# Performance work log

Measured on AMD Instinct MI355X. Metric: run time of the kernel, lower is better.

Reference implementation:

```python
import jax, jax.numpy as jnp
import numpy as np

BITS = 4            # bits per quantized weight
NPACK = 8           # 32-bit container / 4-bit values
CBITS = 32          # compression dtype bit width (int32)
GROUP = 128         # quantization group size along in_features
IN = 4096
OUT = 11008
BATCH = 32


def _dequant(packed_weight, scale):
    # Unpack signed int4 values: (p << (32 - 4*(e+1))) >> 28, arithmetic shift
    # sign-extends, matching the torch recover() path for weight_dtype=int8.
    e = jnp.arange(NPACK, dtype=jnp.int32)                      # [8]
    shifted = (packed_weight[:, :, None] << (CBITS - BITS * (e + 1))) >> (CBITS - BITS)  # [O, I/8, 8]
    w_int = shifted.reshape(OUT, IN).astype(jnp.int8)           # signed int4 in int8
    # Per-group scale: reshape to [O*I/GROUP, GROUP] * [O*I/GROUP, 1]
    w = w_int.astype(jnp.float32).reshape(-1, GROUP) * scale.reshape(-1, 1)
    return w.reshape(OUT, IN)


def setup_inputs() -> dict:
    key = jax.random.key(0)
    k1, k2, k3, k4 = jax.random.split(key, 4)
    x = jax.random.normal(k1, (BATCH, IN), dtype=jnp.float32)
    packed_weight = jax.random.randint(
        k2, (OUT, IN // NPACK), jnp.iinfo(jnp.int32).min, jnp.iinfo(jnp.int32).max,
        dtype=jnp.int32)
    scale = jax.random.uniform(k3, (OUT, IN // GROUP), dtype=jnp.float32,
                               minval=0.001, maxval=0.02)
    bias = jax.random.normal(k4, (OUT,), dtype=jnp.float32)
    return {"x": x, "packed_weight": packed_weight, "scale": scale, "bias": bias}


def reference(x, packed_weight, scale, bias):
    W = _dequant(packed_weight, scale)      # [OUT, IN] fp32
    return x @ W.T + bias                    # F.linear(x, W, bias)
```

## Files before the change

kernel.cpp:

```cpp
#include <hip/hip_runtime.h>

#define IN_F   4096
#define OUT_F  11008
#define BATCH  32
#define NG     32
#define PACKS  512

typedef __bf16 bf16x8_t __attribute__((ext_vector_type(8)));
typedef float  floatx4_t __attribute__((ext_vector_type(4)));

__global__ __launch_bounds__(256) void prep_x(const float* __restrict__ x,
                                              unsigned short* __restrict__ xp) {
  int c  = blockIdx.x * 256 + threadIdx.x;
  int mm = c & 31;
  int k0 = ((c >> 5) & 3) * 32 + ((c >> 7) & 3) * 8 + (c >> 9) * 128;
  const float* src = x + mm * IN_F + k0;
  float4 f0 = *(const float4*)(src);
  float4 f1 = *(const float4*)(src + 4);
  float v[8] = {f0.x, f0.y, f0.z, f0.w, f1.x, f1.y, f1.z, f1.w};
  union { unsigned short s[8]; uint4 u; } r;
#pragma unroll
  for (int j = 0; j < 8; ++j) {
    unsigned int u = __float_as_uint(v[j]);
    unsigned int rnd = ((u >> 16) & 1u) + 0x7fffu;
    r.s[j] = (unsigned short)((u + rnd) >> 16);
  }
  *(uint4*)(xp + c * 8) = r.u;
}

__device__ inline bf16x8_t unpack8(int p) {
  union { unsigned short u[8]; bf16x8_t v; } r;
#pragma unroll
  for (int j = 0; j < 8; ++j) {
    int nib = (p << (28 - 4 * j)) >> 28;
    float f = (float)nib;
    r.u[j] = (unsigned short)(__float_as_uint(f) >> 16);
  }
  return r.v;
}

__device__ inline bf16x8_t load_frag(const unsigned short* p) {
  union { uint4 u; bf16x8_t v; } x;
  x.u = *(const uint4*)p;
  return x.v;
}

__global__ __launch_bounds__(256) void init_out(const float* __restrict__ bias,
                                                float* __restrict__ out) {
  int i = blockIdx.x * 256 + threadIdx.x;
  int e = i << 2;
  int row = e / OUT_F, o = e % OUT_F;
  float4 b = *(const float4*)(bias + o);
  *(float4*)(out + row * OUT_F + o) = b;
}

__global__ __launch_bounds__(256) void wql_part(
    const int* __restrict__ pw, const float* __restrict__ scale,
    const unsigned short* __restrict__ xp, float* __restrict__ out) {
  __shared__ float lds[4][BATCH * 32];

  const int tid = threadIdx.x;
  const int l   = tid & 63;
  const int w   = tid >> 6;
  const int col = l & 15;
  const int q   = l >> 4;
  const int n0  = blockIdx.x * 32;
  const int kc  = blockIdx.y;
  const int nA  = n0 + col;
  const int nB  = n0 + 16 + col;

  floatx4_t acc00 = {0.f, 0.f, 0.f, 0.f};
  floatx4_t acc01 = {0.f, 0.f, 0.f, 0.f};
  floatx4_t acc10 = {0.f, 0.f, 0.f, 0.f};
  floatx4_t acc11 = {0.f, 0.f, 0.f, 0.f};

  const int g0 = kc * 8 + w * 2;
#pragma unroll 1
  for (int gi = 0; gi < 2; ++gi) {
    const int gg = g0 + gi;
    int4 pA = *(const int4*)(pw + nA * PACKS + gg * 16 + q * 4);
    int4 pB = *(const int4*)(pw + nB * PACKS + gg * 16 + q * 4);
    float sA = scale[nA * NG + gg];
    float sB = scale[nB * NG + gg];

    const unsigned short* ab = xp + (gg * 512 + q * 32 + col) * 8;
    bf16x8_t a0[4], a1[4];
#pragma unroll
    for (int t = 0; t < 4; ++t) {
      a0[t] = load_frag(ab + t * 1024);
      a1[t] = load_frag(ab + t * 1024 + 128);
    }

    floatx4_t t00 = {0.f, 0.f, 0.f, 0.f};
    floatx4_t t01 = {0.f, 0.f, 0.f, 0.f};
    floatx4_t t10 = {0.f, 0.f, 0.f, 0.f};
    floatx4_t t11 = {0.f, 0.f, 0.f, 0.f};
    int pAv[4] = {pA.x, pA.y, pA.z, pA.w};
    int pBv[4] = {pB.x, pB.y, pB.z, pB.w};
#pragma unroll
    for (int t = 0; t < 4; ++t) {
      bf16x8_t b0 = unpack8(pAv[t]);
      bf16x8_t b1 = unpack8(pBv[t]);
      t00 = __builtin_amdgcn_mfma_f32_16x16x32_bf16(a0[t], b0, t00, 0, 0, 0);
      t10 = __builtin_amdgcn_mfma_f32_16x16x32_bf16(a1[t], b0, t10, 0, 0, 0);
      t01 = __builtin_amdgcn_mfma_f32_16x16x32_bf16(a0[t], b1, t01, 0, 0, 0);
      t11 = __builtin_amdgcn_mfma_f32_16x16x32_bf16(a1[t], b1, t11, 0, 0, 0);
    }
#pragma unroll
    for (int r = 0; r < 4; ++r) {
      acc00[r] += t00[r] * sA;
      acc10[r] += t10[r] * sA;
      acc01[r] += t01[r] * sB;
      acc11[r] += t11[r] * sB;
    }
  }

#pragma unroll
  for (int r = 0; r < 4; ++r) {
    int row = q * 4 + r;
    lds[w][row * 32 + col]             = acc00[r];
    lds[w][row * 32 + 16 + col]        = acc01[r];
    lds[w][(16 + row) * 32 + col]      = acc10[r];
    lds[w][(16 + row) * 32 + 16 + col] = acc11[r];
  }
  __syncthreads();

  for (int e = tid; e < BATCH * 32; e += 256) {
    int row = e >> 5, cl = e & 31;
    float s = lds[0][e] + lds[1][e] + lds[2][e] + lds[3][e];
    atomicAdd(out + row * OUT_F + n0 + cl, s);
  }
}

extern "C" void kernel_launch(void* const* d_in, const int* in_sizes, int n_in,
                              void* d_out, int out_size, void* d_ws, size_t ws_size,
                              hipStream_t stream) {
  const float* x     = (const float*)d_in[0];
  const int*   pw    = (const int*)d_in[1];
  const float* scale = (const float*)d_in[2];
  const float* bias  = (const float*)d_in[3];
  float* out = (float*)d_out;
  unsigned short* xp = (unsigned short*)d_ws;

  hipLaunchKernelGGL(prep_x, dim3(16384 / 256), dim3(256), 0, stream, x, xp);
  hipLaunchKernelGGL(init_out, dim3((BATCH * OUT_F / 4) / 256), dim3(256), 0,
                     stream, bias, out);
  hipLaunchKernelGGL(wql_part, dim3(OUT_F / 32, 4), dim3(256), 0, stream,
                     pw, scale, xp, out);
}
```

Measured before the change: 86.19 us.

## Replace atomic split-K reduction with partial-sum slices and separate reduce kernel

```diff
diff --git a/kernel.cpp b/kernel.cpp
--- a/kernel.cpp
+++ b/kernel.cpp
@@ -5,6 +5,8 @@
 #define BATCH  32
 #define NG     32
 #define PACKS  512
+#define SLICES 16
+#define SLICE_F (BATCH * OUT_F)
 
 typedef __bf16 bf16x8_t __attribute__((ext_vector_type(8)));
 typedef float  floatx4_t __attribute__((ext_vector_type(4)));
@@ -45,20 +47,9 @@
   return x.v;
 }
 
-__global__ __launch_bounds__(256) void init_out(const float* __restrict__ bias,
-                                                float* __restrict__ out) {
-  int i = blockIdx.x * 256 + threadIdx.x;
-  int e = i << 2;
-  int row = e / OUT_F, o = e % OUT_F;
-  float4 b = *(const float4*)(bias + o);
-  *(float4*)(out + row * OUT_F + o) = b;
-}
-
 __global__ __launch_bounds__(256) void wql_part(
     const int* __restrict__ pw, const float* __restrict__ scale,
-    const unsigned short* __restrict__ xp, float* __restrict__ out) {
-  __shared__ float lds[4][BATCH * 32];
-
+    const unsigned short* __restrict__ xp, float* __restrict__ part) {
   const int tid = threadIdx.x;
   const int l   = tid & 63;
   const int w   = tid >> 6;
@@ -115,21 +106,30 @@
     }
   }
 
+  float* wsp = part + (kc * 4 + w) * SLICE_F + n0;
 #pragma unroll
   for (int r = 0; r < 4; ++r) {
     int row = q * 4 + r;
-    lds[w][row * 32 + col]             = acc00[r];
-    lds[w][row * 32 + 16 + col]        = acc01[r];
-    lds[w][(16 + row) * 32 + col]      = acc10[r];
-    lds[w][(16 + row) * 32 + 16 + col] = acc11[r];
+    wsp[row * OUT_F + col]             = acc00[r];
+    wsp[row * OUT_F + 16 + col]        = acc01[r];
+    wsp[(16 + row) * OUT_F + col]      = acc10[r];
+    wsp[(16 + row) * OUT_F + 16 + col] = acc11[r];
   }
-  __syncthreads();
+}
 
-  for (int e = tid; e < BATCH * 32; e += 256) {
-    int row = e >> 5, cl = e & 31;
-    float s = lds[0][e] + lds[1][e] + lds[2][e] + lds[3][e];
-    atomicAdd(out + row * OUT_F + n0 + cl, s);
+__global__ __launch_bounds__(256) void reduce_out(
+    const float* __restrict__ part, const float* __restrict__ bias,
+    float* __restrict__ out) {
+  int e4 = blockIdx.x * 256 + threadIdx.x;
+  int e  = e4 << 2;
+  int o  = e % OUT_F;
+  float4 s = *(const float4*)(bias + o);
+#pragma unroll
+  for (int k = 0; k < SLICES; ++k) {
+    float4 p = *(const float4*)(part + k * SLICE_F + e);
+    s.x += p.x; s.y += p.y; s.z += p.z; s.w += p.w;
   }
+  *(float4*)(out + e) = s;
 }
 
 extern "C" void kernel_launch(void* const* d_in, const int* in_sizes, int n_in,
@@ -141,10 +141,11 @@
   const float* bias  = (const float*)d_in[3];
   float* out = (float*)d_out;
   unsigned short* xp = (unsigned short*)d_ws;
+  float* part = (float*)((char*)d_ws + (1 << 20));
 
   hipLaunchKernelGGL(prep_x, dim3(16384 / 256), dim3(256), 0, stream, x, xp);
-  hipLaunchKernelGGL(init_out, dim3((BATCH * OUT_F / 4) / 256), dim3(256), 0,
-                     stream, bias, out);
   hipLaunchKernelGGL(wql_part, dim3(OUT_F / 32, 4), dim3(256), 0, stream,
-                     pw, scale, xp, out);
+                     pw, scale, xp, part);
+  hipLaunchKernelGGL(reduce_out, dim3(BATCH * OUT_F / 4 / 256), dim3(256), 0,
+                     stream, part, bias, out);
 }
```

Measured after the change: 89.05 us. 1.03x slower.
